# Optimization experiments

Measured on AMD Instinct MI355X. Metric: run time of the kernel, lower is better.

Reference implementation:

```python
import jax, jax.numpy as jnp
import numpy as np

IMAGE_SIZE = 256
NEAR = 0.1
FAR = 100.0
EPS = 1e-3
BACKGROUND = (0.0, 0.0, 0.0)
CHUNK = 64   # faces per scan step (bounds peak memory of the z-buffer pass)
TINY = 1e-12


def _bary(vx, vy, vz, xp, yp):
    """Barycentric weights / perspective-correct depth at pixel centers.
    vx, vy, vz: 3-tuples of vertex coords, broadcastable with xp/yp.
    Mirrors the CUDA kernel: unnormalized cross-product weights, normalize,
    clamp to [0,1], renormalize, zp = 1 / sum(w_k / z_k), near/far clip."""
    x0, x1, x2 = vx; y0, y1, y2 = vy; z0, z1, z2 = vz
    w0 = yp * (x2 - x1) + xp * (y1 - y2) + (x1 * y2 - x2 * y1)
    w1 = yp * (x0 - x2) + xp * (y2 - y0) + (x2 * y0 - x0 * y2)
    w2 = yp * (x1 - x0) + xp * (y0 - y1) + (x0 * y1 - x1 * y0)
    det = w0 + w1 + w2
    safe_det = jnp.where(jnp.abs(det) > TINY, det, 1.0)
    n0, n1, n2 = w0 / safe_det, w1 / safe_det, w2 / safe_det
    inside = (n0 > 0) & (n1 > 0) & (n2 > 0) & (jnp.abs(det) > TINY)
    n0 = jnp.clip(n0, 0.0, 1.0); n1 = jnp.clip(n1, 0.0, 1.0); n2 = jnp.clip(n2, 0.0, 1.0)
    s = n0 + n1 + n2
    s = jnp.where(s > TINY, s, 1.0)
    n0, n1, n2 = n0 / s, n1 / s, n2 / s
    inv_zp = n0 / z0 + n1 / z1 + n2 / z2
    inv_zp = jnp.where(jnp.abs(inv_zp) > TINY, inv_zp, 1.0)
    zp = 1.0 / inv_zp
    valid = inside & (zp > NEAR) & (zp < FAR)
    return (n0, n1, n2), zp, valid


def _pixel_coords():
    IS = IMAGE_SIZE
    return (2.0 * jnp.arange(IS, dtype=jnp.float32) + 1.0 - IS) / IS


def _forward(faces, textures):
    B, F = faces.shape[:2]
    IS = IMAGE_SIZE
    ii = _pixel_coords()

    # ---- pass 1: z-buffer (face-index argmin), chunked scan over faces ----
    # index selection is non-differentiable -> stop_gradient keeps vjp cheap
    fsg = jax.lax.stop_gradient(faces)
    n_chunks = F // CHUNK
    fchunks = jnp.transpose(fsg.reshape(B, n_chunks, CHUNK, 3, 3), (1, 0, 2, 3, 4))
    bases = jnp.arange(n_chunks, dtype=jnp.int32) * CHUNK
    xp4 = ii[None, None, None, :]
    yp4 = ii[None, None, :, None]

    def step(carry, inp):
        depth, fidx = carry
        fc, base = inp                               # fc: [B, CHUNK, 3, 3]
        vx = tuple(fc[:, :, k, 0][:, :, None, None] for k in range(3))
        vy = tuple(fc[:, :, k, 1][:, :, None, None] for k in range(3))
        vz = tuple(fc[:, :, k, 2][:, :, None, None] for k in range(3))
        _, zp, valid = _bary(vx, vy, vz, xp4, yp4)   # [B, CHUNK, IS, IS]
        zp = jnp.where(valid, zp, jnp.inf)
        local = jnp.argmin(zp, axis=1).astype(jnp.int32)
        zbest = jnp.min(zp, axis=1)
        better = zbest < depth
        depth = jnp.where(better, zbest, depth)
        fidx = jnp.where(better, base + local, fidx)
        return (depth, fidx), None

    init = (jnp.full((B, IS, IS), FAR, jnp.float32),
            jnp.full((B, IS, IS), -1, jnp.int32))
    (_, fidx), _ = jax.lax.scan(step, init, (fchunks, bases))

    # ---- pass 2: differentiable recompute for winning faces ----
    mask = fidx >= 0
    safe_idx = jnp.maximum(fidx, 0)
    fsel = jnp.take_along_axis(
        faces.reshape(B, F, 9), safe_idx.reshape(B, -1, 1), axis=1
    ).reshape(B, IS, IS, 3, 3)
    vx = tuple(fsel[..., k, 0] for k in range(3))
    vy = tuple(fsel[..., k, 1] for k in range(3))
    vz = tuple(fsel[..., k, 2] for k in range(3))
    w, zp, _ = _bary(vx, vy, vz, ii[None, None, :], ii[None, :, None])
    depth_map = jnp.where(mask, zp, FAR)

    # ---- texture sampling: 8-corner trilinear in the T^3 face texel cube ----
    T = textures.shape[2]
    tif = [jnp.clip(w[k] * (T - 1) * zp / vz[k], 0.0, T - 1 - EPS) for k in range(3)]
    lo = [jnp.floor(t) for t in tif]
    fr = [t - l for t, l in zip(tif, lo)]
    lo = [l.astype(jnp.int32) for l in lo]

    tex_flat = textures.reshape(B, F * T * T * T, 3)
    base_idx = safe_idx * (T * T * T)
    rgb = jnp.zeros((B, IS, IS, 3), faces.dtype)
    for d0 in (0, 1):
        for d1 in (0, 1):
            for d2 in (0, 1):
                wgt = ((fr[0] if d0 else 1.0 - fr[0]) *
                       (fr[1] if d1 else 1.0 - fr[1]) *
                       (fr[2] if d2 else 1.0 - fr[2]))
                idx = base_idx + (lo[0] + d0) * T * T + (lo[1] + d1) * T + (lo[2] + d2)
                smp = jnp.take_along_axis(tex_flat, idx.reshape(B, -1, 1), axis=1)
                rgb = rgb + wgt[..., None] * smp.reshape(B, IS, IS, 3)

    bg = jnp.asarray(BACKGROUND, faces.dtype)
    mf = mask.astype(faces.dtype)[..., None]
    rgb_map = rgb * mf + (1.0 - mf) * bg
    alpha_map = mask.astype(faces.dtype)
    # pack (rgb, alpha, depth) into a single [B, IS, IS, 5] tensor
    return jnp.concatenate([rgb_map, alpha_map[..., None], depth_map[..., None]], axis=-1)


def setup_inputs() -> dict:
    key = jax.random.key(0)
    B, F, T = 4, 4096, 4
    k1, k2, k3, k4, k5 = jax.random.split(key, 5)
    # small triangles scattered over the screen with depths in (near, far)
    ctr = jax.random.uniform(k1, (B, F, 1, 2), minval=-0.95, maxval=0.95)
    off = jax.random.uniform(k2, (B, F, 3, 2), minval=-0.08, maxval=0.08)
    xy = ctr + off
    zc = jax.random.uniform(k3, (B, F, 1, 1), minval=1.0, maxval=50.0)
    zo = jax.random.uniform(k4, (B, F, 3, 1), minval=-0.2, maxval=0.2)
    faces = jnp.concatenate([xy, zc + zo], axis=-1).astype(jnp.float32)
    textures = jax.random.uniform(k5, (B, F, T, T, T, 3), dtype=jnp.float32)
    return {"faces": faces, "textures": textures}


def reference(faces, textures):
    return _forward(faces, textures)
```

## Files before the change

### kernel.cpp

```cpp
#include <hip/hip_runtime.h>

#define IS 256
#define FCOUNT 4096
#define NEARP 0.1f
#define FARP 100.0f
#define TINYF 1e-12f
#define CAP 192
#define GCAP 128
#define DET_GLOBAL 1e-5f
#define ZEPS 2e-4f

__device__ __forceinline__ float frn(float r) { asm("" : "+v"(r)); return r; }
__device__ __forceinline__ float mulrn(float a, float b) { return frn(a * b); }
__device__ __forceinline__ float addrn(float a, float b) { return frn(a + b); }
__device__ __forceinline__ float subrn(float a, float b) { return frn(a - b); }
__device__ __forceinline__ float divrn(float a, float b) { return frn(a / b); }
__device__ __forceinline__ float fmarn(float a, float b, float c) {
    return frn(__builtin_fmaf(a, b, c));
}

__global__ __launch_bounds__(64) void bin_kernel(
    const float* __restrict__ faces,
    float4* __restrict__ cA, float4* __restrict__ cB, float4* __restrict__ cC,
    int* __restrict__ counts, int* __restrict__ lists,
    int* __restrict__ gcount, int* __restrict__ glist, int B, int F)
{
    const int gid = blockIdx.x * 64 + threadIdx.x;
    if (gid >= B * F) return;
    const int b = gid >> 12, f = gid & (FCOUNT - 1);
    const float* fp = faces + (size_t)gid * 9;
    const float x0 = fp[0], y0 = fp[1], z0 = fp[2];
    const float x1 = fp[3], y1 = fp[4], z1 = fp[5];
    const float x2 = fp[6], y2 = fp[7], z2 = fp[8];

    const float A0 = subrn(x2, x1), B0 = subrn(y1, y2);
    const float C0 = fmarn(x1, y2, -mulrn(x2, y1));
    const float A1 = subrn(x0, x2), B1 = subrn(y2, y0);
    const float C1 = fmarn(x2, y0, -mulrn(x0, y2));
    const float A2 = subrn(x1, x0), B2 = subrn(y0, y1);
    const float C2 = fmarn(x0, y1, -mulrn(x1, y0));
    cA[gid] = make_float4(A0, B0, C0, A1);
    cB[gid] = make_float4(B1, C1, A2, B2);
    cC[gid] = make_float4(C2, z0, z1, z2);

    const float det = (x1 - x0) * (y2 - y0) - (x2 - x0) * (y1 - y0);
    const float ad = fabsf(det);
    if (ad < DET_GLOBAL) {
        const int pos = atomicAdd(&gcount[b], 1);
        if (pos < GCAP) glist[b * GCAP + pos] = f;
        return;
    }
    const float d = 2e-3f + 3e-7f / ad;
    const float lox = fminf(x0, fminf(x1, x2)) - d;
    const float hix = fmaxf(x0, fmaxf(x1, x2)) + d;
    const float loy = fminf(y0, fminf(y1, y2)) - d;
    const float hiy = fmaxf(y0, fmaxf(y1, y2)) + d;
    int tx0 = (int)ceilf ((256.f * lox + 241.f) * (1.f / 16.f));
    int tx1 = (int)floorf((256.f * hix + 255.f) * (1.f / 16.f));
    int ty0 = (int)ceilf ((256.f * loy + 241.f) * (1.f / 16.f));
    int ty1 = (int)floorf((256.f * hiy + 255.f) * (1.f / 16.f));
    tx0 = max(tx0, 0); tx1 = min(tx1, 31);
    ty0 = max(ty0, 0); ty1 = min(ty1, 31);
    for (int ty = ty0; ty <= ty1; ++ty)
        for (int tx = tx0; tx <= tx1; ++tx) {
            const int t = (b * 32 + ty) * 32 + tx;
            const int pos = atomicAdd(&counts[t], 1);
            if (pos < CAP) lists[(size_t)t * CAP + pos] = f;
        }
}

__global__ __launch_bounds__(256) void raster_kernel(
    const float* __restrict__ faces,
    const float* __restrict__ textures,
    const float4* __restrict__ cA, const float4* __restrict__ cB,
    const float4* __restrict__ cC,
    const int* __restrict__ counts, const int* __restrict__ lists,
    const int* __restrict__ gcount, const int* __restrict__ glist,
    float* __restrict__ out, int B, int F)
{
    const int tid  = threadIdx.x;
    const int lane = tid & 63;
    const int w    = tid >> 6;
    const int b    = blockIdx.x >> 8;
    const int tile = blockIdx.x & 255;
    const int qtx  = 2 * (tile & 15) + (w & 1);
    const int qty  = 2 * (tile >> 4) + (w >> 1);
    const int qbin = (b * 32 + qty) * 32 + qtx;
    const int px   = qtx * 8 + (lane & 7);
    const int py   = qty * 8 + (lane >> 3);
    const float xp = (float)(2 * px + 1 - IS) * (1.0f / IS);
    const float yp = (float)(2 * py + 1 - IS) * (1.0f / IS);

    __shared__ float4 s_a[4][64];
    __shared__ float4 s_b[4][64];
    __shared__ float4 s_c[4][64];
    __shared__ int    s_i[4][64];

    float bestz = FARP;
    int   besti = -1;

    const int cnt  = min(counts[qbin], CAP);
    const int gcnt = min(gcount[b], GCAP);
    const int total = cnt + gcnt;
    const int* mylist = lists + (size_t)qbin * CAP;
    const int* gl     = glist + b * GCAP;
    const int fb = b * F;

    for (int cb = 0; cb < total; cb += 64) {
        const int m = min(total - cb, 64);
        if (lane < m) {
            const int k = cb + lane;
            const int f = (k < cnt) ? mylist[k] : gl[k - cnt];
            s_a[w][lane] = cA[fb + f];
            s_b[w][lane] = cB[fb + f];
            s_c[w][lane] = cC[fb + f];
            s_i[w][lane] = f;
        }
        __builtin_amdgcn_wave_barrier();

        for (int j = 0; j < m; ++j) {
            const float4 fa  = s_a[w][j];
            const float4 fb4 = s_b[w][j];
            const float4 fc  = s_c[w][j];
            const float w0 = addrn(fmarn(yp, fa.x, mulrn(xp, fa.y)), fa.z);
            const float w1 = addrn(fmarn(yp, fa.w, mulrn(xp, fb4.x)), fb4.y);
            const float w2 = addrn(fmarn(yp, fb4.z, mulrn(xp, fb4.w)), fc.x);
            const float det = addrn(addrn(w0, w1), w2);
            bool ins;
            if (det > TINYF)       ins = (w0 > 0.f) && (w1 > 0.f) && (w2 > 0.f);
            else if (det < -TINYF) ins = (w0 < 0.f) && (w1 < 0.f) && (w2 < 0.f);
            else                   ins = false;
            const float minz = fminf(fminf(fc.y, fc.z), fc.w);
            if (ins && minz <= bestz + ZEPS) {
                float n0 = divrn(w0, det), n1 = divrn(w1, det), n2 = divrn(w2, det);
                n0 = frn(fminf(fmaxf(n0, 0.f), 1.f));
                n1 = frn(fminf(fmaxf(n1, 0.f), 1.f));
                n2 = frn(fminf(fmaxf(n2, 0.f), 1.f));
                float s = addrn(addrn(n0, n1), n2);
                s = (s > TINYF) ? s : 1.0f;
                n0 = divrn(n0, s); n1 = divrn(n1, s); n2 = divrn(n2, s);
                float iz = addrn(addrn(divrn(n0, fc.y), divrn(n1, fc.z)),
                                 divrn(n2, fc.w));
                iz = (fabsf(iz) > TINYF) ? iz : 1.0f;
                const float zp = divrn(1.0f, iz);
                if (zp > NEARP && zp < FARP) {
                    const int fi = s_i[w][j];
                    if (zp < bestz || (zp == bestz && fi < besti)) {
                        bestz = zp;
                        besti = fi;
                    }
                }
            }
        }
        __builtin_amdgcn_wave_barrier();
    }

    const float* fbase = faces + (size_t)b * F * 9;
    float r = 0.f, g = 0.f, bch = 0.f, alpha = 0.f, depth = FARP;
    if (besti >= 0) {
        const float* fp = fbase + (size_t)besti * 9;
        const float x0 = fp[0], y0 = fp[1], z0 = fp[2];
        const float x1 = fp[3], y1 = fp[4], z1 = fp[5];
        const float x2 = fp[6], y2 = fp[7], z2 = fp[8];
        const float w0 = addrn(fmarn(yp, subrn(x2, x1), mulrn(xp, subrn(y1, y2))),
                               fmarn(x1, y2, -mulrn(x2, y1)));
        const float w1 = addrn(fmarn(yp, subrn(x0, x2), mulrn(xp, subrn(y2, y0))),
                               fmarn(x2, y0, -mulrn(x0, y2)));
        const float w2 = addrn(fmarn(yp, subrn(x1, x0), mulrn(xp, subrn(y0, y1))),
                               fmarn(x0, y1, -mulrn(x1, y0)));
        const float det = addrn(addrn(w0, w1), w2);
        const float sd = (fabsf(det) > TINYF) ? det : 1.0f;
        float n0 = divrn(w0, sd), n1 = divrn(w1, sd), n2 = divrn(w2, sd);
        n0 = frn(fminf(fmaxf(n0, 0.f), 1.f));
        n1 = frn(fminf(fmaxf(n1, 0.f), 1.f));
        n2 = frn(fminf(fmaxf(n2, 0.f), 1.f));
        float s = addrn(addrn(n0, n1), n2);
        s = (s > TINYF) ? s : 1.0f;
        n0 = divrn(n0, s); n1 = divrn(n1, s); n2 = divrn(n2, s);
        float iz = addrn(addrn(divrn(n0, z0), divrn(n1, z1)), divrn(n2, z2));
        iz = (fabsf(iz) > TINYF) ? iz : 1.0f;
        const float zp = divrn(1.0f, iz);
        depth = zp;

        const float t0 = fminf(fmaxf(divrn(mulrn(mulrn(n0, 3.0f), zp), z0), 0.f), 2.999f);
        const float t1 = fminf(fmaxf(divrn(mulrn(mulrn(n1, 3.0f), zp), z1), 0.f), 2.999f);
        const float t2 = fminf(fmaxf(divrn(mulrn(mulrn(n2, 3.0f), zp), z2), 0.f), 2.999f);
        const float l0 = floorf(t0), l1 = floorf(t1), l2 = floorf(t2);
        const float fr0 = subrn(t0, l0), fr1 = subrn(t1, l1), fr2 = subrn(t2, l2);
        const int i0 = (int)l0, i1 = (int)l1, i2 = (int)l2;

        const float* tx = textures + (size_t)(b * F + besti) * 64 * 3;
        for (int d0 = 0; d0 < 2; ++d0)
            for (int d1 = 0; d1 < 2; ++d1)
                for (int d2 = 0; d2 < 2; ++d2) {
                    const float wg = mulrn(mulrn(d0 ? fr0 : subrn(1.0f, fr0),
                                                 d1 ? fr1 : subrn(1.0f, fr1)),
                                           d2 ? fr2 : subrn(1.0f, fr2));
                    const float* tp = tx + ((i0 + d0) * 16 + (i1 + d1) * 4 + (i2 + d2)) * 3;
                    r   = addrn(r,   mulrn(wg, tp[0]));
                    g   = addrn(g,   mulrn(wg, tp[1]));
                    bch = addrn(bch, mulrn(wg, tp[2]));
                }
        alpha = 1.0f;
    }

    float* op = out + (((size_t)b * IS + py) * IS + px) * 5;
    op[0] = r;
    op[1] = g;
    op[2] = bch;
    op[3] = alpha;
    op[4] = depth;
}

extern "C" void kernel_launch(void* const* d_in, const int* in_sizes, int n_in,
                              void* d_out, int out_size, void* d_ws, size_t ws_size,
                              hipStream_t stream) {
    const float* faces    = (const float*)d_in[0];
    const float* textures = (const float*)d_in[1];
    float* out = (float*)d_out;
    const int F = FCOUNT;
    const int B = in_sizes[0] / (F * 9);
    const int nbins = B * 1024;

    int* counts = (int*)d_ws;
    int* gcount = counts + nbins;
    int* glist  = gcount + B;
    int* lists  = glist + B * GCAP;
    float4* cA  = (float4*)(lists + (size_t)nbins * CAP);
    float4* cB  = cA + (size_t)B * F;
    float4* cC  = cB + (size_t)B * F;

    hipMemsetAsync(counts, 0, (size_t)(nbins + B) * sizeof(int), stream);
    bin_kernel<<<dim3((B * F + 63) / 64), dim3(64), 0, stream>>>(
        faces, cA, cB, cC, counts, lists, gcount, glist, B, F);
    raster_kernel<<<dim3(B * 256), dim3(256), 0, stream>>>(
        faces, textures, cA, cB, cC, counts, lists, gcount, glist, out, B, F);
}
```

Before: 99.57 us.

## Fuse memset, binning and raster into one cooperative kernel with grid syncs

Replaces the memset plus two kernel launches with a single cooperative kernel. It zeroes the bin counters, bins faces with a grid-stride loop, and rasterizes, separating the phases with grid-wide syncs. This removes launch overhead and the inter-kernel gaps. In exchange it adds two grid barriers and requires all 1024 blocks to be co-resident, which a cooperative launch enforces and may fail if occupancy is insufficient.

```diff
diff --git a/kernel.cpp b/kernel.cpp
--- a/kernel.cpp
+++ b/kernel.cpp
@@ -1,4 +1,7 @@
 #include <hip/hip_runtime.h>
+#include <hip/hip_cooperative_groups.h>
+
+namespace cg = cooperative_groups;
 
 #define IS 256
 #define FCOUNT 4096
@@ -19,66 +22,68 @@
     return frn(__builtin_fmaf(a, b, c));
 }
 
-__global__ __launch_bounds__(64) void bin_kernel(
+__global__ __launch_bounds__(256) void fused_kernel(
     const float* __restrict__ faces,
+    const float* __restrict__ textures,
     float4* __restrict__ cA, float4* __restrict__ cB, float4* __restrict__ cC,
     int* __restrict__ counts, int* __restrict__ lists,
-    int* __restrict__ gcount, int* __restrict__ glist, int B, int F)
+    int* __restrict__ gcount, int* __restrict__ glist,
+    float* __restrict__ out, int B, int F, int nbins)
 {
-    const int gid = blockIdx.x * 64 + threadIdx.x;
-    if (gid >= B * F) return;
-    const int b = gid >> 12, f = gid & (FCOUNT - 1);
-    const float* fp = faces + (size_t)gid * 9;
-    const float x0 = fp[0], y0 = fp[1], z0 = fp[2];
-    const float x1 = fp[3], y1 = fp[4], z1 = fp[5];
-    const float x2 = fp[6], y2 = fp[7], z2 = fp[8];
-
-    const float A0 = subrn(x2, x1), B0 = subrn(y1, y2);
-    const float C0 = fmarn(x1, y2, -mulrn(x2, y1));
-    const float A1 = subrn(x0, x2), B1 = subrn(y2, y0);
-    const float C1 = fmarn(x2, y0, -mulrn(x0, y2));
-    const float A2 = subrn(x1, x0), B2 = subrn(y0, y1);
-    const float C2 = fmarn(x0, y1, -mulrn(x1, y0));
-    cA[gid] = make_float4(A0, B0, C0, A1);
-    cB[gid] = make_float4(B1, C1, A2, B2);
-    cC[gid] = make_float4(C2, z0, z1, z2);
-
-    const float det = (x1 - x0) * (y2 - y0) - (x2 - x0) * (y1 - y0);
-    const float ad = fabsf(det);
-    if (ad < DET_GLOBAL) {
-        const int pos = atomicAdd(&gcount[b], 1);
-        if (pos < GCAP) glist[b * GCAP + pos] = f;
-        return;
+    const int tid = threadIdx.x;
+    const int nthreads = gridDim.x * 256;
+    cg::grid_group grid = cg::this_grid();
+
+    for (int zi = blockIdx.x * 256 + tid; zi < nbins + B; zi += nthreads)
+        counts[zi] = 0;
+    __threadfence();
+    grid.sync();
+
+    for (int gid = blockIdx.x * 256 + tid; gid < B * F; gid += nthreads) {
+        const int b = gid >> 12, f = gid & (FCOUNT - 1);
+        const float* fp = faces + (size_t)gid * 9;
+        const float x0 = fp[0], y0 = fp[1], z0 = fp[2];
+        const float x1 = fp[3], y1 = fp[4], z1 = fp[5];
+        const float x2 = fp[6], y2 = fp[7], z2 = fp[8];
+
+        const float A0 = subrn(x2, x1), B0 = subrn(y1, y2);
+        const float C0 = fmarn(x1, y2, -mulrn(x2, y1));
+        const float A1 = subrn(x0, x2), B1 = subrn(y2, y0);
+        const float C1 = fmarn(x2, y0, -mulrn(x0, y2));
+        const float A2 = subrn(x1, x0), B2 = subrn(y0, y1);
+        const float C2 = fmarn(x0, y1, -mulrn(x1, y0));
+        cA[gid] = make_float4(A0, B0, C0, A1);
+        cB[gid] = make_float4(B1, C1, A2, B2);
+        cC[gid] = make_float4(C2, z0, z1, z2);
+
+        const float det = (x1 - x0) * (y2 - y0) - (x2 - x0) * (y1 - y0);
+        const float ad = fabsf(det);
+        if (ad < DET_GLOBAL) {
+            const int pos = atomicAdd(&gcount[b], 1);
+            if (pos < GCAP) glist[b * GCAP + pos] = f;
+            continue;
+        }
+        const float d = 2e-3f + 3e-7f / ad;
+        const float lox = fminf(x0, fminf(x1, x2)) - d;
+        const float hix = fmaxf(x0, fmaxf(x1, x2)) + d;
+        const float loy = fminf(y0, fminf(y1, y2)) - d;
+        const float hiy = fmaxf(y0, fmaxf(y1, y2)) + d;
+        int tx0 = (int)ceilf ((256.f * lox + 241.f) * (1.f / 16.f));
+        int tx1 = (int)floorf((256.f * hix + 255.f) * (1.f / 16.f));
+        int ty0 = (int)ceilf ((256.f * loy + 241.f) * (1.f / 16.f));
+        int ty1 = (int)floorf((256.f * hiy + 255.f) * (1.f / 16.f));
+        tx0 = max(tx0, 0); tx1 = min(tx1, 31);
+        ty0 = max(ty0, 0); ty1 = min(ty1, 31);
+        for (int ty = ty0; ty <= ty1; ++ty)
+            for (int tx = tx0; tx <= tx1; ++tx) {
+                const int t = (b * 32 + ty) * 32 + tx;
+                const int pos = atomicAdd(&counts[t], 1);
+                if (pos < CAP) lists[(size_t)t * CAP + pos] = f;
+            }
     }
-    const float d = 2e-3f + 3e-7f / ad;
-    const float lox = fminf(x0, fminf(x1, x2)) - d;
-    const float hix = fmaxf(x0, fmaxf(x1, x2)) + d;
-    const float loy = fminf(y0, fminf(y1, y2)) - d;
-    const float hiy = fmaxf(y0, fmaxf(y1, y2)) + d;
-    int tx0 = (int)ceilf ((256.f * lox + 241.f) * (1.f / 16.f));
-    int tx1 = (int)floorf((256.f * hix + 255.f) * (1.f / 16.f));
-    int ty0 = (int)ceilf ((256.f * loy + 241.f) * (1.f / 16.f));
-    int ty1 = (int)floorf((256.f * hiy + 255.f) * (1.f / 16.f));
-    tx0 = max(tx0, 0); tx1 = min(tx1, 31);
-    ty0 = max(ty0, 0); ty1 = min(ty1, 31);
-    for (int ty = ty0; ty <= ty1; ++ty)
-        for (int tx = tx0; tx <= tx1; ++tx) {
-            const int t = (b * 32 + ty) * 32 + tx;
-            const int pos = atomicAdd(&counts[t], 1);
-            if (pos < CAP) lists[(size_t)t * CAP + pos] = f;
-        }
-}
-
-__global__ __launch_bounds__(256) void raster_kernel(
-    const float* __restrict__ faces,
-    const float* __restrict__ textures,
-    const float4* __restrict__ cA, const float4* __restrict__ cB,
-    const float4* __restrict__ cC,
-    const int* __restrict__ counts, const int* __restrict__ lists,
-    const int* __restrict__ gcount, const int* __restrict__ glist,
-    float* __restrict__ out, int B, int F)
-{
-    const int tid  = threadIdx.x;
+    __threadfence();
+    grid.sync();
+
     const int lane = tid & 63;
     const int w    = tid >> 6;
     const int b    = blockIdx.x >> 8;
@@ -218,9 +223,9 @@
     const float* faces    = (const float*)d_in[0];
     const float* textures = (const float*)d_in[1];
     float* out = (float*)d_out;
-    const int F = FCOUNT;
-    const int B = in_sizes[0] / (F * 9);
-    const int nbins = B * 1024;
+    int F = FCOUNT;
+    int B = in_sizes[0] / (F * 9);
+    int nbins = B * 1024;
 
     int* counts = (int*)d_ws;
     int* gcount = counts + nbins;
@@ -230,9 +235,12 @@
     float4* cB  = cA + (size_t)B * F;
     float4* cC  = cB + (size_t)B * F;
 
-    hipMemsetAsync(counts, 0, (size_t)(nbins + B) * sizeof(int), stream);
-    bin_kernel<<<dim3((B * F + 63) / 64), dim3(64), 0, stream>>>(
-        faces, cA, cB, cC, counts, lists, gcount, glist, B, F);
-    raster_kernel<<<dim3(B * 256), dim3(256), 0, stream>>>(
-        faces, textures, cA, cB, cC, counts, lists, gcount, glist, out, B, F);
+    void* args[] = {
+        (void*)&faces, (void*)&textures,
+        (void*)&cA, (void*)&cB, (void*)&cC,
+        (void*)&counts, (void*)&lists, (void*)&gcount, (void*)&glist,
+        (void*)&out, (void*)&B, (void*)&F, (void*)&nbins
+    };
+    hipLaunchCooperativeKernel((const void*)fused_kernel,
+                               dim3(B * 256), dim3(256), args, 0, stream);
 }
```

New measurement: 371.2 us. +272.8%, slower.

## Split tile bins into depth buckets and skip far buckets per wave

Applied to the files above, without the earlier changes.

The binning pass now sorts each face into one of four depth buckets per tile, keyed on its minimum vertex depth. The raster pass walks the buckets from near to far. Before each later bucket it takes a wave-wide max of the current best depth and stops once the bucket's lower bound is beyond it. This cuts depth tests on faces that cannot win, at the cost of four times the bin storage, a larger memset, and more small partial chunk loads. Input depths run from about 1 to 50 and triangles are small, so most pixels are covered only by faces in the far bucket, which limits how much gets skipped.

```diff
diff --git a/kernel.cpp b/kernel.cpp
--- a/kernel.cpp
+++ b/kernel.cpp
@@ -9,6 +9,8 @@
 #define GCAP 128
 #define DET_GLOBAL 1e-5f
 #define ZEPS 2e-4f
+
+__device__ __constant__ float BUCKET_LO[4] = {0.0f, 4.0f, 8.0f, 16.0f};
 
 __device__ __forceinline__ float frn(float r) { asm("" : "+v"(r)); return r; }
 __device__ __forceinline__ float mulrn(float a, float b) { return frn(a * b); }
@@ -50,6 +52,9 @@
         if (pos < GCAP) glist[b * GCAP + pos] = f;
         return;
     }
+    const float minz = fminf(z0, fminf(z1, z2));
+    const int bk = (minz < 4.0f) ? 0 : (minz < 8.0f) ? 1 : (minz < 16.0f) ? 2 : 3;
+
     const float d = 2e-3f + 3e-7f / ad;
     const float lox = fminf(x0, fminf(x1, x2)) - d;
     const float hix = fmaxf(x0, fmaxf(x1, x2)) + d;
@@ -64,8 +69,9 @@
     for (int ty = ty0; ty <= ty1; ++ty)
         for (int tx = tx0; tx <= tx1; ++tx) {
             const int t = (b * 32 + ty) * 32 + tx;
-            const int pos = atomicAdd(&counts[t], 1);
-            if (pos < CAP) lists[(size_t)t * CAP + pos] = f;
+            const int slot = t * 4 + bk;
+            const int pos = atomicAdd(&counts[slot], 1);
+            if (pos < CAP) lists[(size_t)slot * CAP + pos] = f;
         }
 }
 
@@ -99,60 +105,75 @@
     float bestz = FARP;
     int   besti = -1;
 
-    const int cnt  = min(counts[qbin], CAP);
+    const int fb = b * F;
     const int gcnt = min(gcount[b], GCAP);
-    const int total = cnt + gcnt;
-    const int* mylist = lists + (size_t)qbin * CAP;
-    const int* gl     = glist + b * GCAP;
-    const int fb = b * F;
-
-    for (int cb = 0; cb < total; cb += 64) {
-        const int m = min(total - cb, 64);
-        if (lane < m) {
-            const int k = cb + lane;
-            const int f = (k < cnt) ? mylist[k] : gl[k - cnt];
-            s_a[w][lane] = cA[fb + f];
-            s_b[w][lane] = cB[fb + f];
-            s_c[w][lane] = cC[fb + f];
-            s_i[w][lane] = f;
+    const int* gl  = glist + b * GCAP;
+
+    for (int seg = 0; seg < 5; ++seg) {
+        int cnt;
+        const int* seglist;
+        if (seg < 4) {
+            if (seg > 0) {
+                float wm = bestz;
+                for (int off = 32; off >= 1; off >>= 1)
+                    wm = fmaxf(wm, __shfl_xor(wm, off));
+                if (BUCKET_LO[seg] > wm + ZEPS) break;
+            }
+            const int slot = qbin * 4 + seg;
+            cnt = min(counts[slot], CAP);
+            seglist = lists + (size_t)slot * CAP;
+        } else {
+            cnt = gcnt;
+            seglist = gl;
         }
-        __builtin_amdgcn_wave_barrier();
-
-        for (int j = 0; j < m; ++j) {
-            const float4 fa  = s_a[w][j];
-            const float4 fb4 = s_b[w][j];
-            const float4 fc  = s_c[w][j];
-            const float w0 = addrn(fmarn(yp, fa.x, mulrn(xp, fa.y)), fa.z);
-            const float w1 = addrn(fmarn(yp, fa.w, mulrn(xp, fb4.x)), fb4.y);
-            const float w2 = addrn(fmarn(yp, fb4.z, mulrn(xp, fb4.w)), fc.x);
-            const float det = addrn(addrn(w0, w1), w2);
-            bool ins;
-            if (det > TINYF)       ins = (w0 > 0.f) && (w1 > 0.f) && (w2 > 0.f);
-            else if (det < -TINYF) ins = (w0 < 0.f) && (w1 < 0.f) && (w2 < 0.f);
-            else                   ins = false;
-            const float minz = fminf(fminf(fc.y, fc.z), fc.w);
-            if (ins && minz <= bestz + ZEPS) {
-                float n0 = divrn(w0, det), n1 = divrn(w1, det), n2 = divrn(w2, det);
-                n0 = frn(fminf(fmaxf(n0, 0.f), 1.f));
-                n1 = frn(fminf(fmaxf(n1, 0.f), 1.f));
-                n2 = frn(fminf(fmaxf(n2, 0.f), 1.f));
-                float s = addrn(addrn(n0, n1), n2);
-                s = (s > TINYF) ? s : 1.0f;
-                n0 = divrn(n0, s); n1 = divrn(n1, s); n2 = divrn(n2, s);
-                float iz = addrn(addrn(divrn(n0, fc.y), divrn(n1, fc.z)),
-                                 divrn(n2, fc.w));
-                iz = (fabsf(iz) > TINYF) ? iz : 1.0f;
-                const float zp = divrn(1.0f, iz);
-                if (zp > NEARP && zp < FARP) {
-                    const int fi = s_i[w][j];
-                    if (zp < bestz || (zp == bestz && fi < besti)) {
-                        bestz = zp;
-                        besti = fi;
+
+        for (int cb = 0; cb < cnt; cb += 64) {
+            const int m = min(cnt - cb, 64);
+            if (lane < m) {
+                const int f = seglist[cb + lane];
+                s_a[w][lane] = cA[fb + f];
+                s_b[w][lane] = cB[fb + f];
+                s_c[w][lane] = cC[fb + f];
+                s_i[w][lane] = f;
+            }
+            __builtin_amdgcn_wave_barrier();
+
+            for (int j = 0; j < m; ++j) {
+                const float4 fa  = s_a[w][j];
+                const float4 fb4 = s_b[w][j];
+                const float4 fc  = s_c[w][j];
+                const float w0 = addrn(fmarn(yp, fa.x, mulrn(xp, fa.y)), fa.z);
+                const float w1 = addrn(fmarn(yp, fa.w, mulrn(xp, fb4.x)), fb4.y);
+                const float w2 = addrn(fmarn(yp, fb4.z, mulrn(xp, fb4.w)), fc.x);
+                const float det = addrn(addrn(w0, w1), w2);
+                bool ins;
+                if (det > TINYF)       ins = (w0 > 0.f) && (w1 > 0.f) && (w2 > 0.f);
+                else if (det < -TINYF) ins = (w0 < 0.f) && (w1 < 0.f) && (w2 < 0.f);
+                else                   ins = false;
+                const float minz = fminf(fminf(fc.y, fc.z), fc.w);
+                if (ins && minz <= bestz + ZEPS) {
+                    float n0 = divrn(w0, det), n1 = divrn(w1, det), n2 = divrn(w2, det);
+                    n0 = frn(fminf(fmaxf(n0, 0.f), 1.f));
+                    n1 = frn(fminf(fmaxf(n1, 0.f), 1.f));
+                    n2 = frn(fminf(fmaxf(n2, 0.f), 1.f));
+                    float s = addrn(addrn(n0, n1), n2);
+                    s = (s > TINYF) ? s : 1.0f;
+                    n0 = divrn(n0, s); n1 = divrn(n1, s); n2 = divrn(n2, s);
+                    float iz = addrn(addrn(divrn(n0, fc.y), divrn(n1, fc.z)),
+                                     divrn(n2, fc.w));
+                    iz = (fabsf(iz) > TINYF) ? iz : 1.0f;
+                    const float zp = divrn(1.0f, iz);
+                    if (zp > NEARP && zp < FARP) {
+                        const int fi = s_i[w][j];
+                        if (zp < bestz || (zp == bestz && fi < besti)) {
+                            bestz = zp;
+                            besti = fi;
+                        }
                     }
                 }
             }
+            __builtin_amdgcn_wave_barrier();
         }
-        __builtin_amdgcn_wave_barrier();
     }
 
     const float* fbase = faces + (size_t)b * F * 9;
@@ -221,16 +242,17 @@
     const int F = FCOUNT;
     const int B = in_sizes[0] / (F * 9);
     const int nbins = B * 1024;
+    const int nslots = nbins * 4;
 
     int* counts = (int*)d_ws;
-    int* gcount = counts + nbins;
+    int* gcount = counts + nslots;
     int* glist  = gcount + B;
     int* lists  = glist + B * GCAP;
-    float4* cA  = (float4*)(lists + (size_t)nbins * CAP);
+    float4* cA  = (float4*)(lists + (size_t)nslots * CAP);
     float4* cB  = cA + (size_t)B * F;
     float4* cC  = cB + (size_t)B * F;
 
-    hipMemsetAsync(counts, 0, (size_t)(nbins + B) * sizeof(int), stream);
+    hipMemsetAsync(counts, 0, (size_t)(nslots + B) * sizeof(int), stream);
     bin_kernel<<<dim3((B * F + 63) / 64), dim3(64), 0, stream>>>(
         faces, cA, cB, cC, counts, lists, gcount, glist, B, F);
     raster_kernel<<<dim3(B * 256), dim3(256), 0, stream>>>(
```

Measured after the change: 99.87 us. No clear change (+0.3%).
